# Performance work log

Hardware: AMD Instinct MI355X
Metric: run time of the kernel (lower is better)

Reference implementation:

```python
import jax, jax.numpy as jnp
import numpy as np


def setup_inputs() -> dict:
    key = jax.random.key(0)
    ks = jax.random.split(key, 8)
    N, E, D, MAX_NODES, C = 100000, 1536, 128, 250000, 2
    embeddings = jax.random.normal(ks[0], (N, E), dtype=jnp.float32)
    node_ids = jnp.arange(N, dtype=jnp.int64)  # default global_ids path
    # persistent node memory buffer (warm state mid-sequence)
    memory = jax.random.normal(ks[1], (MAX_NODES, D), dtype=jnp.float32) * 0.1
    s_ih = 1.0 / np.sqrt(E)
    s_hh = 1.0 / np.sqrt(D)
    w_ih = jax.random.normal(ks[2], (3 * D, E), dtype=jnp.float32) * s_ih
    w_hh = jax.random.normal(ks[3], (3 * D, D), dtype=jnp.float32) * s_hh
    b_ih = jax.random.normal(ks[4], (3 * D,), dtype=jnp.float32) * s_hh
    b_hh = jax.random.normal(ks[5], (3 * D,), dtype=jnp.float32) * s_hh
    s_c = 1.0 / np.sqrt(E + D)
    cls_w = jax.random.normal(ks[6], (C, E + D), dtype=jnp.float32) * s_c
    cls_b = jax.random.normal(ks[7], (C,), dtype=jnp.float32) * s_c
    return {"embeddings": embeddings, "node_ids": node_ids, "memory": memory,
            "w_ih": w_ih, "w_hh": w_hh, "b_ih": b_ih, "b_hh": b_hh,
            "cls_w": cls_w, "cls_b": cls_b}


def reference(embeddings, node_ids, memory, w_ih, w_hh, b_ih, b_hh, cls_w, cls_b):
    # gather previous memory rows for the active nodes: [N, D]
    prev = memory[node_ids]
    # torch.nn.GRUCell math
    gi = embeddings @ w_ih.T + b_ih  # [N, 3D]
    gh = prev @ w_hh.T + b_hh        # [N, 3D]
    i_r, i_z, i_n = jnp.split(gi, 3, axis=1)
    h_r, h_z, h_n = jnp.split(gh, 3, axis=1)
    r = jax.nn.sigmoid(i_r + h_r)
    z = jax.nn.sigmoid(i_z + h_z)
    n = jnp.tanh(i_n + r * h_n)
    new_mem = (1.0 - z) * n + z * prev  # [N, D]
    # scatter updated rows back into the persistent buffer (detached in torch)
    updated_memory = memory.at[node_ids].set(jax.lax.stop_gradient(new_mem))
    # classifier on [embeddings ; new_mem]; dropout is identity in eval
    combined = jnp.concatenate([embeddings, new_mem], axis=1)
    logits = combined @ cls_w.T + cls_b  # [N, 2]
    return logits, updated_memory
```

## Files before the change

kernel.cpp:

```cpp
#include <hip/hip_runtime.h>
#include <hip/hip_bf16.h>

typedef __bf16 bf16;
typedef __bf16 bf16x4 __attribute__((ext_vector_type(4)));
typedef __bf16 bf16x8 __attribute__((ext_vector_type(8)));
typedef float  f32x4  __attribute__((ext_vector_type(4)));

#define EDIM 1536
#define DDIM 128
#define CDIM 1664
#define TM   64
#define NCH  48

#define MFMA_B16(a, b, c) __builtin_amdgcn_mfma_f32_16x16x32_bf16((a), (b), (c), 0, 0, 0)

__device__ __forceinline__ float sigf(float x) { return 1.0f / (1.0f + __expf(-x)); }
__device__ __forceinline__ float tanhf_fast(float x) { return 2.0f / (1.0f + __expf(-2.0f * x)) - 1.0f; }

__device__ __forceinline__ void glds16(const void* g, void* l) {
  __builtin_amdgcn_global_load_lds(
      (const __attribute__((address_space(1))) unsigned int*)g,
      (__attribute__((address_space(3))) unsigned int*)l, 16, 0, 0);
}

template <int LDA>
__device__ __forceinline__ void stageW(const bf16* __restrict__ w, int k0,
                                       char* dst, int wave, int lane) {
#pragma unroll
  for (int j = 0; j < 3; ++j) {
    const int segbase = j * 512 + wave * 64;
    const int s = segbase + lane;
    const int n = ((s >> 6) << 4) + (s & 15);
    const int q = (s >> 4) & 3;
    glds16(w + (size_t)n * LDA + k0 + q * 8, dst + (size_t)segbase * 16);
  }
}

__global__ __launch_bounds__(256) void prep_convert(const float* __restrict__ w_ih,
                                                    const float* __restrict__ w_hh,
                                                    bf16* __restrict__ wib,
                                                    bf16* __restrict__ whb) {
  const int i = (blockIdx.x * 256 + threadIdx.x) * 4;
  const int TIH = 3 * DDIM * EDIM;
  const int THH = 3 * DDIM * DDIM;
  if (i < TIH) {
    const float4 v = *(const float4*)(w_ih + i);
    bf16x4 o = {(bf16)v.x, (bf16)v.y, (bf16)v.z, (bf16)v.w};
    *(bf16x4*)(wib + i) = o;
  } else if (i < TIH + THH) {
    const int j = i - TIH;
    const float4 v = *(const float4*)(w_hh + j);
    bf16x4 o = {(bf16)v.x, (bf16)v.y, (bf16)v.z, (bf16)v.w};
    *(bf16x4*)(whb + j) = o;
  }
}

__global__ __launch_bounds__(512, 4) void gru_fused(
    const float* __restrict__ emb, const int* __restrict__ ids,
    const float* __restrict__ mem,
    const float* __restrict__ b_ih, const float* __restrict__ b_hh,
    const float* __restrict__ cls_w, const float* __restrict__ cls_b,
    const bf16* __restrict__ wib, const bf16* __restrict__ whb,
    float* __restrict__ logits, float* __restrict__ omem, int Nrows)
{
  __shared__ char  sW[2][24576];
  __shared__ char  sA[2][5120];
  __shared__ char  sP[16384];
  __shared__ float sLp[64][2];
  __shared__ int   sIds[64];

  const int t    = threadIdx.x;
  const int lane = t & 63;
  const int wave = t >> 6;
  const int wm   = wave >> 2;
  const int wn   = wave & 3;
  const int l15  = lane & 15;
  const int lq   = lane >> 4;
  const int m0   = blockIdx.x * TM;

  if (t < 64)  sIds[t] = (m0 + t < Nrows) ? ids[m0 + t] : 0;
  if (t < 128) sLp[t >> 1][t & 1] = cls_b[t & 1];

  f32x4 accR[2][2], accZ[2][2], accN[2][2], accH[2][2];
#pragma unroll
  for (int sub = 0; sub < 2; ++sub) {
    const int nc = wn * 32 + sub * 16 + l15;
    const float br = b_ih[nc] + b_hh[nc];
    const float bz = b_ih[128 + nc] + b_hh[128 + nc];
    const float bn = b_ih[256 + nc];
    const float bh = b_hh[256 + nc];
#pragma unroll
    for (int mt = 0; mt < 2; ++mt) {
      accR[mt][sub] = (f32x4){br, br, br, br};
      accZ[mt][sub] = (f32x4){bz, bz, bz, bz};
      accN[mt][sub] = (f32x4){bn, bn, bn, bn};
      accH[mt][sub] = (f32x4){bh, bh, bh, bh};
    }
  }

  const int wrd = (wn << 11) + (lq << 8) + (l15 << 4);

  const int  ar = t >> 3;
  const int  aq = t & 7;
  const bool av = (m0 + ar) < Nrows;
  const float* pA = emb + (size_t)(m0 + ar) * EDIM + aq * 4;
  const int  awofs = ar * 80 + aq * 8;
  float lp0 = 0.f, lp1 = 0.f;

  stageW<EDIM>(wib, 0, sW[0], wave, lane);
  {
    float4 a = make_float4(0.f, 0.f, 0.f, 0.f);
    if (av) a = *(const float4*)pA;
    const float4 c0 = *(const float4*)(cls_w + aq * 4);
    const float4 c1 = *(const float4*)(cls_w + CDIM + aq * 4);
    lp0 += a.x * c0.x + a.y * c0.y + a.z * c0.z + a.w * c0.w;
    lp1 += a.x * c1.x + a.y * c1.y + a.z * c1.z + a.w * c1.w;
    bf16x4 o = {(bf16)a.x, (bf16)a.y, (bf16)a.z, (bf16)a.w};
    *(bf16x4*)(sA[0] + awofs) = o;
  }
  __syncthreads();

  for (int s = 0; s < NCH; ++s) {
    const int cur = s & 1, nxt = cur ^ 1;
    const bool pf = (s + 1) < NCH;
    if (pf) stageW<EDIM>(wib, (s + 1) * 32, sW[nxt], wave, lane);

    bf16x8 af[2];
#pragma unroll
    for (int mt = 0; mt < 2; ++mt) {
      const int m = wm * 32 + mt * 16 + l15;
      af[mt] = *(bf16x8*)(sA[cur] + m * 80 + lq * 16);
    }
#pragma unroll
    for (int g = 0; g < 3; ++g) {
#pragma unroll
      for (int sub = 0; sub < 2; ++sub) {
        const bf16x8 bfr = *(bf16x8*)(sW[cur] + (((g << 3) + sub) << 10) + wrd);
        if (g == 0) {
          accR[0][sub] = MFMA_B16(af[0], bfr, accR[0][sub]);
          accR[1][sub] = MFMA_B16(af[1], bfr, accR[1][sub]);
        } else if (g == 1) {
          accZ[0][sub] = MFMA_B16(af[0], bfr, accZ[0][sub]);
          accZ[1][sub] = MFMA_B16(af[1], bfr, accZ[1][sub]);
        } else {
          accN[0][sub] = MFMA_B16(af[0], bfr, accN[0][sub]);
          accN[1][sub] = MFMA_B16(af[1], bfr, accN[1][sub]);
        }
      }
    }
    if (pf) {
      const int kn = (s + 1) * 32;
      float4 a = make_float4(0.f, 0.f, 0.f, 0.f);
      if (av) a = *(const float4*)(pA + kn);
      const float4 c0 = *(const float4*)(cls_w + kn + aq * 4);
      const float4 c1 = *(const float4*)(cls_w + CDIM + kn + aq * 4);
      lp0 += a.x * c0.x + a.y * c0.y + a.z * c0.z + a.w * c0.w;
      lp1 += a.x * c1.x + a.y * c1.y + a.z * c1.z + a.w * c1.w;
      bf16x4 o = {(bf16)a.x, (bf16)a.y, (bf16)a.z, (bf16)a.w};
      *(bf16x4*)(sA[nxt] + awofs) = o;
    }
    __syncthreads();
  }

  {
    float v0 = lp0, v1 = lp1;
    v0 += __shfl_xor(v0, 1); v0 += __shfl_xor(v0, 2); v0 += __shfl_xor(v0, 4);
    v1 += __shfl_xor(v1, 1); v1 += __shfl_xor(v1, 2); v1 += __shfl_xor(v1, 4);
    if ((lane & 7) == 0) {
      atomicAdd(&sLp[ar][0], v0);
      atomicAdd(&sLp[ar][1], v1);
    }
  }

  stageW<DDIM>(whb, 0, sW[0], wave, lane);
  {
    const int prow = t >> 5;
    const int pc   = t & 31;
#pragma unroll
    for (int p = 0; p < 4; ++p) {
      const int r = p * 16 + prow;
      const float4 v = *(const float4*)(mem + (size_t)sIds[r] * DDIM + pc * 4);
      bf16x4 o = {(bf16)v.x, (bf16)v.y, (bf16)v.z, (bf16)v.w};
      *(bf16x4*)(sP + r * 256 + ((pc << 3) ^ ((r & 7) << 4))) = o;
    }
  }
  __syncthreads();

  for (int ks = 0; ks < 4; ++ks) {
    const int cur = ks & 1, nxt = cur ^ 1;
    if (ks + 1 < 4) stageW<DDIM>(whb, (ks + 1) * 32, sW[nxt], wave, lane);
    bf16x8 af[2];
#pragma unroll
    for (int mt = 0; mt < 2; ++mt) {
      const int m = wm * 32 + mt * 16 + l15;
      const int kb = (ks * 32 + lq * 8) << 1;
      af[mt] = *(bf16x8*)(sP + m * 256 + (kb ^ ((m & 7) << 4)));
    }
#pragma unroll
    for (int g = 0; g < 3; ++g) {
#pragma unroll
      for (int sub = 0; sub < 2; ++sub) {
        const bf16x8 bfr = *(bf16x8*)(sW[cur] + (((g << 3) + sub) << 10) + wrd);
        if (g == 0) {
          accR[0][sub] = MFMA_B16(af[0], bfr, accR[0][sub]);
          accR[1][sub] = MFMA_B16(af[1], bfr, accR[1][sub]);
        } else if (g == 1) {
          accZ[0][sub] = MFMA_B16(af[0], bfr, accZ[0][sub]);
          accZ[1][sub] = MFMA_B16(af[1], bfr, accZ[1][sub]);
        } else {
          accH[0][sub] = MFMA_B16(af[0], bfr, accH[0][sub]);
          accH[1][sub] = MFMA_B16(af[1], bfr, accH[1][sub]);
        }
      }
    }
    __syncthreads();
  }

  float lpM[8][2];
#pragma unroll
  for (int i = 0; i < 8; ++i) { lpM[i][0] = 0.f; lpM[i][1] = 0.f; }

#pragma unroll
  for (int mt = 0; mt < 2; ++mt) {
#pragma unroll
    for (int sub = 0; sub < 2; ++sub) {
      const int d = wn * 32 + sub * 16 + l15;
      const float cw0 = cls_w[EDIM + d];
      const float cw1 = cls_w[CDIM + EDIM + d];
#pragma unroll
      for (int j = 0; j < 4; ++j) {
        const int m = wm * 32 + mt * 16 + lq * 4 + j;
        const float r = sigf(accR[mt][sub][j]);
        const float z = sigf(accZ[mt][sub][j]);
        const float n = tanhf_fast(accN[mt][sub][j] + r * accH[mt][sub][j]);
        const float pv = mem[(size_t)sIds[m] * DDIM + d];
        const float nv = (1.0f - z) * n + z * pv;
        if (m0 + m < Nrows) omem[(size_t)sIds[m] * DDIM + d] = nv;
        lpM[mt * 4 + j][0] += nv * cw0;
        lpM[mt * 4 + j][1] += nv * cw1;
      }
    }
  }

#pragma unroll
  for (int i = 0; i < 8; ++i) {
#pragma unroll
    for (int c = 0; c < 2; ++c) {
      float v = lpM[i][c];
      v += __shfl_xor(v, 1); v += __shfl_xor(v, 2);
      v += __shfl_xor(v, 4); v += __shfl_xor(v, 8);
      if (l15 == 0) {
        const int m = wm * 32 + (i >> 2) * 16 + lq * 4 + (i & 3);
        atomicAdd(&sLp[m][c], v);
      }
    }
  }
  __syncthreads();

  if (t < 128) {
    const int m = t >> 1, c = t & 1;
    if (m0 + m < Nrows) logits[(size_t)(m0 + m) * 2 + c] = sLp[m][c];
  }
}

extern "C" void kernel_launch(void* const* d_in, const int* in_sizes, int n_in,
                              void* d_out, int out_size, void* d_ws, size_t ws_size,
                              hipStream_t stream) {
  const float* emb   = (const float*)d_in[0];
  const int*   ids   = (const int*)d_in[1];
  const float* mem   = (const float*)d_in[2];
  const float* w_ih  = (const float*)d_in[3];
  const float* w_hh  = (const float*)d_in[4];
  const float* b_ih  = (const float*)d_in[5];
  const float* b_hh  = (const float*)d_in[6];
  const float* cls_w = (const float*)d_in[7];
  const float* cls_b = (const float*)d_in[8];

  const int N    = in_sizes[0] / EDIM;
  const int MAXN = in_sizes[2] / DDIM;

  float* logits = (float*)d_out;
  float* omem   = (float*)d_out + (size_t)N * 2;
  bf16*  wib    = (bf16*)d_ws;
  bf16*  whb    = wib + 3 * DDIM * EDIM;

  hipMemcpyAsync(omem, mem, (size_t)MAXN * DDIM * sizeof(float),
                 hipMemcpyDeviceToDevice, stream);
  const int prep_threads = (3 * DDIM * EDIM + 3 * DDIM * DDIM) / 4;
  prep_convert<<<(prep_threads + 255) / 256, 256, 0, stream>>>(w_ih, w_hh, wib, whb);
  gru_fused<<<(N + TM - 1) / TM, 512, 0, stream>>>(emb, ids, mem, b_ih, b_hh,
                                                   cls_w, cls_b, wib, whb,
                                                   logits, omem, N);
}
```

Baseline: 517.5 us.

## Halve row tile to 32, remap waves over columns, prefetch embeddings two chunks ahead

Cuts the per-block row tile from 64 to 32. The eight waves now split the 128 hidden columns, each wave computing one 16-column slice for all 32 rows, and the weight staging layout is changed to a plain row-major layout. The embedding tile in LDS is XOR-swizzled, and the embedding loads are software-pipelined two chunks ahead in registers so global latency is hidden behind the MFMAs. The intent is better latency hiding and more blocks in flight. The cost is that each block reuses the staged weights over half as many rows, so weight traffic into LDS per row doubles, and there are twice as many barriers per row.

```diff
diff --git a/kernel.cpp b/kernel.cpp
--- a/kernel.cpp
+++ b/kernel.cpp
@@ -2,6 +2,7 @@
 #include <hip/hip_bf16.h>
 
 typedef __bf16 bf16;
+typedef __bf16 bf16x2 __attribute__((ext_vector_type(2)));
 typedef __bf16 bf16x4 __attribute__((ext_vector_type(4)));
 typedef __bf16 bf16x8 __attribute__((ext_vector_type(8)));
 typedef float  f32x4  __attribute__((ext_vector_type(4)));
@@ -9,8 +10,8 @@
 #define EDIM 1536
 #define DDIM 128
 #define CDIM 1664
-#define TM   64
-#define NCH  48
+#define TM   32
+#define NCHA 48
 
 #define MFMA_B16(a, b, c) __builtin_amdgcn_mfma_f32_16x16x32_bf16((a), (b), (c), 0, 0, 0)
 
@@ -30,8 +31,8 @@
   for (int j = 0; j < 3; ++j) {
     const int segbase = j * 512 + wave * 64;
     const int s = segbase + lane;
-    const int n = ((s >> 6) << 4) + (s & 15);
-    const int q = (s >> 4) & 3;
+    const int n = s >> 2;
+    const int q = s & 3;
     glds16(w + (size_t)n * LDA + k0 + q * 8, dst + (size_t)segbase * 16);
   }
 }
@@ -64,121 +65,123 @@
     float* __restrict__ logits, float* __restrict__ omem, int Nrows)
 {
   __shared__ char  sW[2][24576];
-  __shared__ char  sA[2][5120];
-  __shared__ char  sP[16384];
-  __shared__ float sLp[64][2];
-  __shared__ int   sIds[64];
+  __shared__ char  sA[2][4096];
+  __shared__ char  sP[8192];
+  __shared__ float sLp[32][2];
+  __shared__ int   sIds[32];
 
   const int t    = threadIdx.x;
   const int lane = t & 63;
   const int wave = t >> 6;
-  const int wm   = wave >> 2;
   const int wn   = wave & 3;
+  const int ws   = wave >> 2;
   const int l15  = lane & 15;
   const int lq   = lane >> 4;
   const int m0   = blockIdx.x * TM;
 
-  if (t < 64)  sIds[t] = (m0 + t < Nrows) ? ids[m0 + t] : 0;
-  if (t < 128) sLp[t >> 1][t & 1] = cls_b[t & 1];
-
-  f32x4 accR[2][2], accZ[2][2], accN[2][2], accH[2][2];
-#pragma unroll
-  for (int sub = 0; sub < 2; ++sub) {
-    const int nc = wn * 32 + sub * 16 + l15;
+  if (t < 32) sIds[t] = (m0 + t < Nrows) ? ids[m0 + t] : 0;
+  if (t < 64) sLp[t >> 1][t & 1] = cls_b[t & 1];
+
+  const int nc = wn * 32 + ws * 16 + l15;
+  f32x4 accR[2], accZ[2], accN[2], accH[2];
+  {
     const float br = b_ih[nc] + b_hh[nc];
     const float bz = b_ih[128 + nc] + b_hh[128 + nc];
     const float bn = b_ih[256 + nc];
     const float bh = b_hh[256 + nc];
 #pragma unroll
     for (int mt = 0; mt < 2; ++mt) {
-      accR[mt][sub] = (f32x4){br, br, br, br};
-      accZ[mt][sub] = (f32x4){bz, bz, bz, bz};
-      accN[mt][sub] = (f32x4){bn, bn, bn, bn};
-      accH[mt][sub] = (f32x4){bh, bh, bh, bh};
-    }
-  }
-
-  const int wrd = (wn << 11) + (lq << 8) + (l15 << 4);
-
-  const int  ar = t >> 3;
-  const int  aq = t & 7;
-  const bool av = (m0 + ar) < Nrows;
-  const float* pA = emb + (size_t)(m0 + ar) * EDIM + aq * 4;
-  const int  awofs = ar * 80 + aq * 8;
+      accR[mt] = (f32x4){br, br, br, br};
+      accZ[mt] = (f32x4){bz, bz, bz, bz};
+      accN[mt] = (f32x4){bn, bn, bn, bn};
+      accH[mt] = (f32x4){bh, bh, bh, bh};
+    }
+  }
+
+  const int  arow = t >> 4;
+  const int  ac2  = (t & 15) * 2;
+  const bool av   = (m0 + arow) < Nrows;
+  const float* pA = emb + (size_t)(m0 + arow) * EDIM + ac2;
+  const int  awofs = arow * 128 + ((ac2 * 2) ^ ((arow & 7) << 4));
   float lp0 = 0.f, lp1 = 0.f;
+  float2 aE = make_float2(0.f, 0.f), aO = aE;
+
+#define STOREA(BUF, AR) do {                                   \
+    bf16x2 o_ = {(bf16)(AR).x, (bf16)(AR).y};                  \
+    *(bf16x2*)(sA[BUF] + awofs) = o_;                          \
+  } while (0)
 
   stageW<EDIM>(wib, 0, sW[0], wave, lane);
   {
-    float4 a = make_float4(0.f, 0.f, 0.f, 0.f);
-    if (av) a = *(const float4*)pA;
-    const float4 c0 = *(const float4*)(cls_w + aq * 4);
-    const float4 c1 = *(const float4*)(cls_w + CDIM + aq * 4);
-    lp0 += a.x * c0.x + a.y * c0.y + a.z * c0.z + a.w * c0.w;
-    lp1 += a.x * c1.x + a.y * c1.y + a.z * c1.z + a.w * c1.w;
-    bf16x4 o = {(bf16)a.x, (bf16)a.y, (bf16)a.z, (bf16)a.w};
-    *(bf16x4*)(sA[0] + awofs) = o;
+    float2 p = av ? *(const float2*)pA : make_float2(0.f, 0.f);
+    const float2 c0 = *(const float2*)(cls_w + ac2);
+    const float2 c1 = *(const float2*)(cls_w + CDIM + ac2);
+    lp0 += p.x * c0.x + p.y * c0.y;
+    lp1 += p.x * c1.x + p.y * c1.y;
+    STOREA(0, p);
+    if (av) {
+      aE = *(const float2*)(pA + 32);
+      aO = *(const float2*)(pA + 64);
+    }
   }
   __syncthreads();
 
-  for (int s = 0; s < NCH; ++s) {
-    const int cur = s & 1, nxt = cur ^ 1;
-    const bool pf = (s + 1) < NCH;
-    if (pf) stageW<EDIM>(wib, (s + 1) * 32, sW[nxt], wave, lane);
-
-    bf16x8 af[2];
-#pragma unroll
-    for (int mt = 0; mt < 2; ++mt) {
-      const int m = wm * 32 + mt * 16 + l15;
-      af[mt] = *(bf16x8*)(sA[cur] + m * 80 + lq * 16);
-    }
-#pragma unroll
-    for (int g = 0; g < 3; ++g) {
-#pragma unroll
-      for (int sub = 0; sub < 2; ++sub) {
-        const bf16x8 bfr = *(bf16x8*)(sW[cur] + (((g << 3) + sub) << 10) + wrd);
-        if (g == 0) {
-          accR[0][sub] = MFMA_B16(af[0], bfr, accR[0][sub]);
-          accR[1][sub] = MFMA_B16(af[1], bfr, accR[1][sub]);
-        } else if (g == 1) {
-          accZ[0][sub] = MFMA_B16(af[0], bfr, accZ[0][sub]);
-          accZ[1][sub] = MFMA_B16(af[1], bfr, accZ[1][sub]);
-        } else {
-          accN[0][sub] = MFMA_B16(af[0], bfr, accN[0][sub]);
-          accN[1][sub] = MFMA_B16(af[1], bfr, accN[1][sub]);
-        }
-      }
-    }
-    if (pf) {
-      const int kn = (s + 1) * 32;
-      float4 a = make_float4(0.f, 0.f, 0.f, 0.f);
-      if (av) a = *(const float4*)(pA + kn);
-      const float4 c0 = *(const float4*)(cls_w + kn + aq * 4);
-      const float4 c1 = *(const float4*)(cls_w + CDIM + kn + aq * 4);
-      lp0 += a.x * c0.x + a.y * c0.y + a.z * c0.z + a.w * c0.w;
-      lp1 += a.x * c1.x + a.y * c1.y + a.z * c1.z + a.w * c1.w;
-      bf16x4 o = {(bf16)a.x, (bf16)a.y, (bf16)a.z, (bf16)a.w};
-      *(bf16x4*)(sA[nxt] + awofs) = o;
-    }
-    __syncthreads();
-  }
+#define BODYA(C, AR) do {                                                      \
+    const int cur_ = (C) & 1, nxt_ = cur_ ^ 1;                                 \
+    const bool pf_ = (C) + 1 < NCHA;                                           \
+    if (pf_) stageW<EDIM>(wib, ((C) + 1) * 32, sW[nxt_], wave, lane);          \
+    float2 c0_, c1_;                                                           \
+    if (pf_) {                                                                 \
+      c0_ = *(const float2*)(cls_w + ((C) + 1) * 32 + ac2);                    \
+      c1_ = *(const float2*)(cls_w + CDIM + ((C) + 1) * 32 + ac2);             \
+    }                                                                          \
+    bf16x8 af0_ = *(bf16x8*)(sA[cur_] + (l15) * 128 +                          \
+                             ((lq * 16) ^ ((l15 & 7) << 4)));                  \
+    bf16x8 af1_ = *(bf16x8*)(sA[cur_] + (16 + l15) * 128 +                     \
+                             ((lq * 16) ^ ((l15 & 7) << 4)));                  \
+    const bf16x8 bR_ = *(bf16x8*)(sW[cur_] + (nc      ) * 64 + lq * 16);       \
+    const bf16x8 bZ_ = *(bf16x8*)(sW[cur_] + (nc + 128) * 64 + lq * 16);       \
+    const bf16x8 bN_ = *(bf16x8*)(sW[cur_] + (nc + 256) * 64 + lq * 16);       \
+    accR[0] = MFMA_B16(af0_, bR_, accR[0]);                                    \
+    accR[1] = MFMA_B16(af1_, bR_, accR[1]);                                    \
+    accZ[0] = MFMA_B16(af0_, bZ_, accZ[0]);                                    \
+    accZ[1] = MFMA_B16(af1_, bZ_, accZ[1]);                                    \
+    accN[0] = MFMA_B16(af0_, bN_, accN[0]);                                    \
+    accN[1] = MFMA_B16(af1_, bN_, accN[1]);                                    \
+    if (pf_) {                                                                 \
+      lp0 += (AR).x * c0_.x + (AR).y * c0_.y;                                  \
+      lp1 += (AR).x * c1_.x + (AR).y * c1_.y;                                  \
+      STOREA(nxt_, AR);                                                        \
+    }                                                                          \
+    if ((C) + 3 < NCHA && av) AR = *(const float2*)(pA + ((C) + 3) * 32);      \
+    __syncthreads();                                                           \
+  } while (0)
+
+  for (int c2 = 0; c2 < NCHA; c2 += 2) {
+    BODYA(c2,     aE);
+    BODYA(c2 + 1, aO);
+  }
+#undef BODYA
 
   {
     float v0 = lp0, v1 = lp1;
-    v0 += __shfl_xor(v0, 1); v0 += __shfl_xor(v0, 2); v0 += __shfl_xor(v0, 4);
-    v1 += __shfl_xor(v1, 1); v1 += __shfl_xor(v1, 2); v1 += __shfl_xor(v1, 4);
-    if ((lane & 7) == 0) {
-      atomicAdd(&sLp[ar][0], v0);
-      atomicAdd(&sLp[ar][1], v1);
+    v0 += __shfl_xor(v0, 1); v0 += __shfl_xor(v0, 2);
+    v0 += __shfl_xor(v0, 4); v0 += __shfl_xor(v0, 8);
+    v1 += __shfl_xor(v1, 1); v1 += __shfl_xor(v1, 2);
+    v1 += __shfl_xor(v1, 4); v1 += __shfl_xor(v1, 8);
+    if (l15 == 0) {
+      atomicAdd(&sLp[arow][0], v0);
+      atomicAdd(&sLp[arow][1], v1);
     }
   }
 
   stageW<DDIM>(whb, 0, sW[0], wave, lane);
-  {
+  if (t < 256) {
     const int prow = t >> 5;
     const int pc   = t & 31;
 #pragma unroll
     for (int p = 0; p < 4; ++p) {
-      const int r = p * 16 + prow;
+      const int r = p * 8 + prow;
       const float4 v = *(const float4*)(mem + (size_t)sIds[r] * DDIM + pc * 4);
       bf16x4 o = {(bf16)v.x, (bf16)v.y, (bf16)v.z, (bf16)v.w};
       *(bf16x4*)(sP + r * 256 + ((pc << 3) ^ ((r & 7) << 4))) = o;
@@ -186,81 +189,72 @@
   }
   __syncthreads();
 
+#pragma unroll
   for (int ks = 0; ks < 4; ++ks) {
     const int cur = ks & 1, nxt = cur ^ 1;
     if (ks + 1 < 4) stageW<DDIM>(whb, (ks + 1) * 32, sW[nxt], wave, lane);
     bf16x8 af[2];
 #pragma unroll
     for (int mt = 0; mt < 2; ++mt) {
-      const int m = wm * 32 + mt * 16 + l15;
+      const int m = mt * 16 + l15;
       const int kb = (ks * 32 + lq * 8) << 1;
       af[mt] = *(bf16x8*)(sP + m * 256 + (kb ^ ((m & 7) << 4)));
     }
-#pragma unroll
-    for (int g = 0; g < 3; ++g) {
-#pragma unroll
-      for (int sub = 0; sub < 2; ++sub) {
-        const bf16x8 bfr = *(bf16x8*)(sW[cur] + (((g << 3) + sub) << 10) + wrd);
-        if (g == 0) {
-          accR[0][sub] = MFMA_B16(af[0], bfr, accR[0][sub]);
-          accR[1][sub] = MFMA_B16(af[1], bfr, accR[1][sub]);
-        } else if (g == 1) {
-          accZ[0][sub] = MFMA_B16(af[0], bfr, accZ[0][sub]);
-          accZ[1][sub] = MFMA_B16(af[1], bfr, accZ[1][sub]);
-        } else {
-          accH[0][sub] = MFMA_B16(af[0], bfr, accH[0][sub]);
-          accH[1][sub] = MFMA_B16(af[1], bfr, accH[1][sub]);
-        }
-      }
-    }
+    const bf16x8 bR = *(bf16x8*)(sW[cur] + (nc      ) * 64 + lq * 16);
+    const bf16x8 bZ = *(bf16x8*)(sW[cur] + (nc + 128) * 64 + lq * 16);
+    const bf16x8 bH = *(bf16x8*)(sW[cur] + (nc + 256) * 64 + lq * 16);
+    accR[0] = MFMA_B16(af[0], bR, accR[0]);
+    accR[1] = MFMA_B16(af[1], bR, accR[1]);
+    accZ[0] = MFMA_B16(af[0], bZ, accZ[0]);
+    accZ[1] = MFMA_B16(af[1], bZ, accZ[1]);
+    accH[0] = MFMA_B16(af[0], bH, accH[0]);
+    accH[1] = MFMA_B16(af[1], bH, accH[1]);
     __syncthreads();
   }
 
-  float lpM[8][2];
-#pragma unroll
-  for (int i = 0; i < 8; ++i) { lpM[i][0] = 0.f; lpM[i][1] = 0.f; }
-
-#pragma unroll
-  for (int mt = 0; mt < 2; ++mt) {
-#pragma unroll
-    for (int sub = 0; sub < 2; ++sub) {
-      const int d = wn * 32 + sub * 16 + l15;
-      const float cw0 = cls_w[EDIM + d];
-      const float cw1 = cls_w[CDIM + EDIM + d];
+  {
+    const int d = nc;
+    const float cw0 = cls_w[EDIM + d];
+    const float cw1 = cls_w[CDIM + EDIM + d];
+    float lpm[8][2];
+#pragma unroll
+    for (int i = 0; i < 8; ++i) { lpm[i][0] = 0.f; lpm[i][1] = 0.f; }
+#pragma unroll
+    for (int mt = 0; mt < 2; ++mt) {
 #pragma unroll
       for (int j = 0; j < 4; ++j) {
-        const int m = wm * 32 + mt * 16 + lq * 4 + j;
-        const float r = sigf(accR[mt][sub][j]);
-        const float z = sigf(accZ[mt][sub][j]);
-        const float n = tanhf_fast(accN[mt][sub][j] + r * accH[mt][sub][j]);
+        const int m = mt * 16 + lq * 4 + j;
+        const float r = sigf(accR[mt][j]);
+        const float z = sigf(accZ[mt][j]);
+        const float n = tanhf_fast(accN[mt][j] + r * accH[mt][j]);
         const float pv = mem[(size_t)sIds[m] * DDIM + d];
         const float nv = (1.0f - z) * n + z * pv;
         if (m0 + m < Nrows) omem[(size_t)sIds[m] * DDIM + d] = nv;
-        lpM[mt * 4 + j][0] += nv * cw0;
-        lpM[mt * 4 + j][1] += nv * cw1;
+        lpm[mt * 4 + j][0] += nv * cw0;
+        lpm[mt * 4 + j][1] += nv * cw1;
       }
     }
-  }
-
-#pragma unroll
-  for (int i = 0; i < 8; ++i) {
-#pragma unroll
-    for (int c = 0; c < 2; ++c) {
-      float v = lpM[i][c];
-      v += __shfl_xor(v, 1); v += __shfl_xor(v, 2);
-      v += __shfl_xor(v, 4); v += __shfl_xor(v, 8);
-      if (l15 == 0) {
-        const int m = wm * 32 + (i >> 2) * 16 + lq * 4 + (i & 3);
-        atomicAdd(&sLp[m][c], v);
+#pragma unroll
+    for (int i = 0; i < 8; ++i) {
+#pragma unroll
+      for (int c = 0; c < 2; ++c) {
+        float v = lpm[i][c];
+        v += __shfl_xor(v, 1); v += __shfl_xor(v, 2);
+        v += __shfl_xor(v, 4); v += __shfl_xor(v, 8);
+        if (l15 == 0) {
+          const int m = (i >> 2) * 16 + lq * 4 + (i & 3);
+          atomicAdd(&sLp[m][c], v);
+        }
       }
     }
   }
   __syncthreads();
 
-  if (t < 128) {
+  if (t < 64) {
     const int m = t >> 1, c = t & 1;
     if (m0 + m < Nrows) logits[(size_t)(m0 + m) * 2 + c] = sLp[m][c];
   }
+#undef STOREA
 }
 
 extern "C" void kernel_launch(void* const* d_in, const int* in_sizes, int n_in,
```

Result: slower. 577.1 us (+11.5%).
